# Kernel optimization log

Hardware: AMD Instinct MI355X
Metric: run time of the kernel (lower is better)

## Reference

```python
import jax, jax.numpy as jnp
import numpy as np

TEMPERATURE = 0.8
TOP_K = 50
TOP_P = 0.9
REP_PENALTY = 1.2
NEG_INF = -1000000000.0


def setup_inputs() -> dict:
    key = jax.random.key(0)
    k1, k2 = jax.random.split(key)
    B, S, V, L = 64, 8, 50257, 2048
    logits = jax.random.normal(k1, (B, S, V), dtype=jnp.float32)
    input_ids = jax.random.randint(k2, (B, L), 0, V, dtype=jnp.int64)
    return {"logits": logits, "input_ids": input_ids}


def _modify_logits(logits, input_ids):
    B, S, V = logits.shape
    # temperature scale
    x = logits / TEMPERATURE
    # top-k: keep values >= k-th largest (ties negligible for random floats)
    kth = jax.lax.top_k(x, TOP_K)[0][..., -1:]  # [B,S,1]
    x = jnp.where(x >= kth, x, NEG_INF)
    # top-p nucleus filtering
    order = jnp.argsort(-x, axis=-1)                       # descending order indices
    sorted_logits = jnp.take_along_axis(x, order, axis=-1)
    cum = jnp.cumsum(jax.nn.softmax(sorted_logits, axis=-1), axis=-1)
    remove = cum > TOP_P
    # shift right by one; always keep the top token
    remove = jnp.concatenate([jnp.zeros_like(remove[..., :1]), remove[..., :-1]], axis=-1)
    inv = jnp.argsort(order, axis=-1)                      # inverse permutation
    remove_orig = jnp.take_along_axis(remove, inv, axis=-1)
    x = jnp.where(remove_orig, NEG_INF, x)
    # repetition penalty on last position only, for tokens present in history
    present = jnp.zeros((B, V), dtype=bool).at[
        jnp.arange(B)[:, None], input_ids
    ].set(True)
    last = x[:, -1, :]
    penalized = jnp.where(last < 0, last * REP_PENALTY, last / REP_PENALTY)
    last = jnp.where(present, penalized, last)
    return x.at[:, -1, :].set(last)


def reference(logits, input_ids):
    return _modify_logits(logits, input_ids)
```

## Files before the change

### kernel.cpp

```cpp
#include <hip/hip_runtime.h>
#include <stdint.h>

#define V 50257
#define B_ 64
#define S_ 8
#define ROWS (B_ * S_)
#define L_ 2048
#define NEG_INF -1000000000.0f
#define PEN_NEG (-1200000000.0f)
#define MASK_WORDS_PER_B 1571
#define TOTAL (ROWS * V)
#define NVEC (TOTAL / 4)
#define TOP_CAP 64
#define TRAW 2.8f
#define F4L 7
#define WCHUNK_F4 (64 * F4L)
#define ELEMS_PER_WAVE (WCHUNK_F4 * 4)
#define NWAVES ((NVEC + WCHUNK_F4 - 1) / WCHUNK_F4)
#define GW_BLOCKS ((NWAVES + 3) / 4)
#define WCAP 32
#define CAPROW 512

#define WS_WCNT    0
#define WS_GCAND   65536
#define WS_NEED    (WS_GCAND + (size_t)NWAVES * WCAP * 8)
#define WS_ROWPARAM 0
#define WS_MASK     8192

__device__ __forceinline__ unsigned fkey(float f) {
    unsigned u = __float_as_uint(f);
    return (u & 0x80000000u) ? ~u : (u | 0x80000000u);
}

__device__ __forceinline__ int blockReduceSum256(int v, int tid, int* s4) {
#pragma unroll
    for (int off = 32; off; off >>= 1) v += __shfl_down(v, off);
    __syncthreads();
    if ((tid & 63) == 0) s4[tid >> 6] = v;
    __syncthreads();
    return s4[0] + s4[1] + s4[2] + s4[3];
}


__global__ __launch_bounds__(256) void gather_kernel(const float4* __restrict__ in4,
                                                     uint2* __restrict__ gcand,
                                                     unsigned* __restrict__ wcnt) {
    const int wid = blockIdx.x * 4 + (threadIdx.x >> 6);
    if (wid >= NWAVES) return;
    const int lane = threadIdx.x & 63;
    const int b = wid * WCHUNK_F4 + lane;

    const float4* p0 = in4 + min(b,          NVEC - 1);
    const float4* p1 = in4 + min(b + 64,     NVEC - 1);
    const float4* p2 = in4 + min(b + 2 * 64, NVEC - 1);
    const float4* p3 = in4 + min(b + 3 * 64, NVEC - 1);
    const float4* p4 = in4 + min(b + 4 * 64, NVEC - 1);
    const float4* p5 = in4 + min(b + 5 * 64, NVEC - 1);
    const float4* p6 = in4 + min(b + 6 * 64, NVEC - 1);

    float4 va0, va1, va2, va3, va4, va5, va6;
#define LOADPIN(dst, src)                                                     \
    asm volatile("global_load_dwordx4 %0, %1, off" : "=v"(dst) : "v"(src));   \
    __builtin_amdgcn_sched_barrier(0);
    LOADPIN(va0, p0) LOADPIN(va1, p1) LOADPIN(va2, p2) LOADPIN(va3, p3)
    LOADPIN(va4, p4) LOADPIN(va5, p5) LOADPIN(va6, p6)
#undef LOADPIN
    asm volatile("s_waitcnt vmcnt(0)" ::: "memory");
    __builtin_amdgcn_sched_barrier(0);

    float q0v = 0.f, q1v = 0.f, q2v = 0.f, q3v = 0.f, q4v = 0.f, q5v = 0.f, q6v = 0.f, q7v = 0.f;
    int q0i = 0, q1i = 0, q2i = 0, q3i = 0, q4i = 0, q5i = 0, q6i = 0, q7i = 0;
    int nh = 0;

#define INS(val, ei)                                                          \
    if ((val) >= TRAW) {                                                      \
        q7v = q6v; q7i = q6i; q6v = q5v; q6i = q5i; q5v = q4v; q5i = q4i;     \
        q4v = q3v; q4i = q3i; q3v = q2v; q3i = q2i; q2v = q1v; q2i = q1i;     \
        q1v = q0v; q1i = q0i; q0v = (val); q0i = (ei); ++nh;                  \
    }
#define CONSUME(vv, kk)                                                       \
    {                                                                         \
        int i = b + (kk) * 64;                                                \
        if (i < NVEC) {                                                       \
            int e = i << 2;                                                   \
            INS((vv).x, e)                                                    \
            INS((vv).y, e + 1)                                                \
            INS((vv).z, e + 2)                                                \
            INS((vv).w, e + 3)                                                \
        }                                                                     \
    }
    CONSUME(va0, 0) CONSUME(va1, 1) CONSUME(va2, 2) CONSUME(va3, 3)
    CONSUME(va4, 4) CONSUME(va5, 5) CONSUME(va6, 6)
#undef CONSUME
#undef INS

    int m = nh > 8 ? 8 : nh;
    int incl = m;
#pragma unroll
    for (int d = 1; d < 64; d <<= 1) {
        int t = __shfl_up(incl, d);
        if (lane >= d) incl += t;
    }
    int excl = incl - m;
    int total = __shfl(incl, 63);
    bool of = (total > WCAP) || __any(nh > 8);

    size_t rb = (size_t)wid * WCAP;
    if (m >= 1 && excl + 0 < WCAP) gcand[rb + excl + 0] = make_uint2((unsigned)q0i, __float_as_uint(q0v));
    if (m >= 2 && excl + 1 < WCAP) gcand[rb + excl + 1] = make_uint2((unsigned)q1i, __float_as_uint(q1v));
    if (m >= 3 && excl + 2 < WCAP) gcand[rb + excl + 2] = make_uint2((unsigned)q2i, __float_as_uint(q2v));
    if (m >= 4 && excl + 3 < WCAP) gcand[rb + excl + 3] = make_uint2((unsigned)q3i, __float_as_uint(q3v));
    if (m >= 5 && excl + 4 < WCAP) gcand[rb + excl + 4] = make_uint2((unsigned)q4i, __float_as_uint(q4v));
    if (m >= 6 && excl + 5 < WCAP) gcand[rb + excl + 5] = make_uint2((unsigned)q5i, __float_as_uint(q5v));
    if (m >= 7 && excl + 6 < WCAP) gcand[rb + excl + 6] = make_uint2((unsigned)q6i, __float_as_uint(q6v));
    if (m >= 8 && excl + 7 < WCAP) gcand[rb + excl + 7] = make_uint2((unsigned)q7i, __float_as_uint(q7v));
    if (lane == 0) wcnt[wid] = of ? 1000000u : (unsigned)total;
}


__global__ __launch_bounds__(256) void select_kernel(const float* __restrict__ logits,
                                                     const int* __restrict__ ids,
                                                     const uint2* __restrict__ gcand,
                                                     const unsigned* __restrict__ wcnt,
                                                     float* __restrict__ out) {
    const int row = blockIdx.x;
    const int tid = threadIdx.x;
    __shared__ float cX[CAPROW];
    __shared__ unsigned cR[CAPROW];
    __shared__ int cI[CAPROW];
    __shared__ float sVal[TOP_CAP];
    __shared__ int sIdx[TOP_CAP];
    __shared__ double sExp[TOP_CAP];
    __shared__ unsigned presRow[MASK_WORDS_PER_B];
    __shared__ unsigned s_wc[40];
    __shared__ int s_c, s_M, s_bad, s_ti;
    __shared__ float s_t;
    __shared__ int s_red[4];

    const float* rp = logits + (size_t)row * V;
    const unsigned e0 = (unsigned)row * (unsigned)V;
    if (tid == 0) { s_c = 0; s_bad = 0; }
    __syncthreads();

    {
        const int r0 = (int)(e0 / (unsigned)ELEMS_PER_WAVE);
        const int r1 = (int)((e0 + V - 1) / (unsigned)ELEMS_PER_WAVE);
        const int nr = r1 - r0 + 1;
        if (tid < nr) s_wc[tid] = wcnt[r0 + tid];
        __syncthreads();
        const int nslots = nr * WCAP;
        for (int j = tid; j < nslots; j += 256) {
            int r = j >> 5;
            int sl = j & 31;
            unsigned c = s_wc[r];
            if (c > (unsigned)WCAP) { s_bad = 1; c = WCAP; }
            if (sl < (int)c) {
                uint2 u = gcand[(size_t)(r0 + r) * WCAP + sl];
                if (u.x / (unsigned)V == (unsigned)row) {
                    int p = atomicAdd(&s_c, 1);
                    if (p < CAPROW) {
                        cR[p] = u.y;
                        cX[p] = __uint_as_float(u.y) / 0.8f;
                        cI[p] = (int)(u.x - e0);
                    }
                }
            }
        }
    }
    __syncthreads();
    int cnt = s_c;
    if (s_bad || cnt < 50 || cnt > CAPROW) {
        unsigned lo = 0u, hi = 0xFFFFFFFFu;
        while (lo < hi) {
            unsigned mid = lo + ((hi - lo) >> 1) + 1u;
            int c = 0;
            for (int j = tid; j < V; j += 256) c += (int)(fkey(rp[j]) >= mid);
            c = blockReduceSum256(c, tid, s_red);
            if (c >= 50) lo = mid; else hi = mid - 1u;
        }
        unsigned gl = (lo > 2u) ? lo - 2u : 0u;
        __syncthreads();
        if (tid == 0) s_c = 0;
        __syncthreads();
        for (int j = tid; j < V; j += 256) {
            float v = rp[j];
            if (fkey(v) >= gl) {
                int p = atomicAdd(&s_c, 1);
                if (p < CAPROW) { cR[p] = __float_as_uint(v); cX[p] = v / 0.8f; cI[p] = j; }
            }
        }
        __syncthreads();
        cnt = min(s_c, CAPROW);
    }

    if (tid < TOP_CAP) { sVal[tid] = -3.4e38f; sIdx[tid] = 0x7FFFFFFF; }
    __syncthreads();

    {
        float v0 = -3.4e38f, v1 = -3.4e38f;
        int i0 = 0x7FFFFFFF, i1 = 0x7FFFFFFF;
        if (tid < cnt) { v0 = cX[tid]; i0 = cI[tid]; }
        if (tid + 256 < cnt) { v1 = cX[tid + 256]; i1 = cI[tid + 256]; }
        int r0 = 0, r1 = 0;
        for (int j = 0; j < cnt; ++j) {
            float w = cX[j];
            int wi = cI[j];
            r0 += (w > v0) || (w == v0 && wi < i0);
            r1 += (w > v1) || (w == v1 && wi < i1);
        }
        if (tid < cnt && r0 < TOP_CAP) { sVal[r0] = v0; sIdx[r0] = i0; }
        if (tid + 256 < cnt && r1 < TOP_CAP) { sVal[r1] = v1; sIdx[r1] = i1; }
    }
    __syncthreads();

    if (tid == 0) {
        float kth = sVal[49];
        int M = 50;
        while (M < TOP_CAP && sVal[M] == kth) ++M;
        s_M = M;
    }
    __syncthreads();
    int M = s_M;
    if (tid < M) sExp[tid] = exp((double)sVal[tid] - (double)sVal[0]);
    __syncthreads();
    if (tid == 0) {
        double denom = 0.0;
        for (int i = 0; i < M; ++i) denom += sExp[i];
        double cum = 0.0;
        int J = M - 1;
        for (int i = 0; i < M; ++i) {
            cum += sExp[i] / denom;
            if (cum > 0.9) { J = i; break; }
        }
        s_t = sVal[J];
        s_ti = sIdx[J];
    }

    const bool pen = (row & 7) == 7;
    if (pen) {
        __syncthreads();
        for (int w = tid; w < MASK_WORDS_PER_B; w += 256) presRow[w] = 0u;
        __syncthreads();
        const int* bp = ids + (row >> 3) * L_;
#pragma unroll
        for (int k = 0; k < L_ / 256; ++k) {
            int t = bp[k * 256 + tid];
            atomicOr(&presRow[t >> 5], 1u << (t & 31));
        }
    }
    __syncthreads();

    float* orow = out + (size_t)row * V;
    const unsigned mis = (unsigned)(((size_t)row * (size_t)V) & 3u);
    const int a0 = (int)((4u - mis) & 3u);
    const int nv = (V - a0) >> 2;
    const int tailStart = a0 + (nv << 2);
    if (tid < a0) {
        int t = tid;
        orow[t] = (pen && ((presRow[t >> 5] >> (t & 31)) & 1u)) ? PEN_NEG : NEG_INF;
    }
    if (tid < V - tailStart) {
        int t = tailStart + tid;
        orow[t] = (pen && ((presRow[t >> 5] >> (t & 31)) & 1u)) ? PEN_NEG : NEG_INF;
    }
    float4* ob = reinterpret_cast<float4*>(orow + a0);
    if (!pen) {
        const float4 bg = make_float4(NEG_INF, NEG_INF, NEG_INF, NEG_INF);
        for (int j = tid; j < nv; j += 256) ob[j] = bg;
    } else {
        for (int j = tid; j < nv; j += 256) {
            int t = a0 + (j << 2);
            float4 bg;
            bg.x = ((presRow[t >> 5]     >> (t & 31))     & 1u) ? PEN_NEG : NEG_INF;
            bg.y = ((presRow[(t+1) >> 5] >> ((t+1) & 31)) & 1u) ? PEN_NEG : NEG_INF;
            bg.z = ((presRow[(t+2) >> 5] >> ((t+2) & 31)) & 1u) ? PEN_NEG : NEG_INF;
            bg.w = ((presRow[(t+3) >> 5] >> ((t+3) & 31)) & 1u) ? PEN_NEG : NEG_INF;
            ob[j] = bg;
        }
    }
    __syncthreads();

    float t = s_t;
    int tie = s_ti;
    for (int j = tid; j < cnt; j += 256) {
        float x = cX[j];
        int tok = cI[j];
        bool keep = (x > t) || (x == t && tok <= tie);
        if (keep) {
            float oo = x;
            if (pen && ((presRow[tok >> 5] >> (tok & 31)) & 1u))
                oo = (oo < 0.0f) ? oo * 1.2f : oo * (1.0f / 1.2f);
            orow[tok] = oo;
        }
    }
}

#define CAND_CAP 4096
#define RT_THREADS 1024

__global__ __launch_bounds__(256) void mask_only_kernel(const int* __restrict__ ids,
                                                        unsigned* __restrict__ mask) {
    const int tid = threadIdx.x;
    const int b = blockIdx.x;
    __shared__ unsigned lds[MASK_WORDS_PER_B];
    for (int w = tid; w < MASK_WORDS_PER_B; w += 256) lds[w] = 0u;
    __syncthreads();
    const int* bp = ids + b * L_;
#pragma unroll
    for (int k = 0; k < L_ / 256; ++k) {
        int t = bp[k * 256 + tid];
        atomicOr(&lds[t >> 5], 1u << (t & 31));
    }
    __syncthreads();
    unsigned* mp = mask + b * MASK_WORDS_PER_B;
    for (int w = tid; w < MASK_WORDS_PER_B; w += 256) mp[w] = lds[w];
}

__global__ __launch_bounds__(RT_THREADS, 8) void row_thresh_kernel(
        const float* __restrict__ logits, uint4* __restrict__ rowParam) {
    const int tid = threadIdx.x;
    const int row = blockIdx.x;
    if (row >= ROWS) return;
    const float* rp = logits + (size_t)row * V;

    __shared__ float candV[CAND_CAP];
    __shared__ int   candI[CAND_CAP];
    __shared__ float sVal[TOP_CAP];
    __shared__ int   sIdx[TOP_CAP];
    __shared__ double sExp[TOP_CAP];
    __shared__ int s_cnt, s_M;
    __shared__ int s_red[RT_THREADS / 64];

    const unsigned mis = (unsigned)(((size_t)row * (size_t)V) & 3u);
    const int a0 = (int)((4u - mis) & 3u);
    const int nv = (V - a0) >> 2;
    const int tailStart = a0 + (nv << 2);
    const float4* vp = reinterpret_cast<const float4*>(rp + a0);

    float TR = 2.4f;
    int cnt = 0;
    for (int attempt = 0; attempt < 12; ++attempt) {
        if (tid == 0) s_cnt = 0;
        __syncthreads();
        for (int base = tid; base < nv; base += 4 * RT_THREADS) {
            int i1 = base + RT_THREADS, i2 = base + 2 * RT_THREADS, i3 = base + 3 * RT_THREADS;
            float4 a = vp[base];
            float4 b = vp[i1 < nv ? i1 : nv - 1];
            float4 c = vp[i2 < nv ? i2 : nv - 1];
            float4 d = vp[i3 < nv ? i3 : nv - 1];
            float va[16] = {a.x, a.y, a.z, a.w, b.x, b.y, b.z, b.w,
                            c.x, c.y, c.z, c.w, d.x, d.y, d.z, d.w};
            int ib[4] = {base, i1, i2, i3};
            bool ok[4] = {true, i1 < nv, i2 < nv, i3 < nv};
#pragma unroll
            for (int q = 0; q < 4; ++q) {
                if (!ok[q]) continue;
#pragma unroll
                for (int cc = 0; cc < 4; ++cc) {
                    float v = va[q * 4 + cc];
                    if (v >= TR) {
                        int p = atomicAdd(&s_cnt, 1);
                        if (p < CAND_CAP) { candV[p] = v / 0.8f; candI[p] = a0 + (ib[q] << 2) + cc; }
                    }
                }
            }
        }
        if (tid < a0) {
            float v = rp[tid];
            if (v >= TR) {
                int p = atomicAdd(&s_cnt, 1);
                if (p < CAND_CAP) { candV[p] = v / 0.8f; candI[p] = tid; }
            }
        }
        if (tid < V - tailStart) {
            float v = rp[tailStart + tid];
            if (v >= TR) {
                int p = atomicAdd(&s_cnt, 1);
                if (p < CAND_CAP) { candV[p] = v / 0.8f; candI[p] = tailStart + tid; }
            }
        }
        __syncthreads();
        cnt = s_cnt;
        if (cnt >= 50 && cnt <= CAND_CAP) break;
        if (cnt < 50) TR -= 1.2f; else TR += 1.2f;
        __syncthreads();
    }
    if (cnt > CAND_CAP) cnt = CAND_CAP;

    if (tid < TOP_CAP) { sVal[tid] = -3.4e38f; sIdx[tid] = 0x7FFFFFFF; }
    __syncthreads();

    {
        float v0 = (tid < cnt) ? candV[tid] : -3.4e38f;
        int i0 = (tid < cnt) ? candI[tid] : 0x7FFFFFFF;
        float v1 = (tid + RT_THREADS < cnt) ? candV[tid + RT_THREADS] : -3.4e38f;
        int i1 = (tid + RT_THREADS < cnt) ? candI[tid + RT_THREADS] : 0x7FFFFFFF;
        float v2 = (tid + 2 * RT_THREADS < cnt) ? candV[tid + 2 * RT_THREADS] : -3.4e38f;
        int i2 = (tid + 2 * RT_THREADS < cnt) ? candI[tid + 2 * RT_THREADS] : 0x7FFFFFFF;
        float v3 = (tid + 3 * RT_THREADS < cnt) ? candV[tid + 3 * RT_THREADS] : -3.4e38f;
        int i3 = (tid + 3 * RT_THREADS < cnt) ? candI[tid + 3 * RT_THREADS] : 0x7FFFFFFF;
        int r0 = 0, r1 = 0, r2 = 0, r3 = 0;
        for (int j = 0; j < cnt; ++j) {
            float w = candV[j];
            int wi = candI[j];
            r0 += (w > v0) || (w == v0 && wi < i0);
            r1 += (w > v1) || (w == v1 && wi < i1);
            r2 += (w > v2) || (w == v2 && wi < i2);
            r3 += (w > v3) || (w == v3 && wi < i3);
        }
        if (tid < cnt && r0 < TOP_CAP) { sVal[r0] = v0; sIdx[r0] = i0; }
        if (tid + RT_THREADS < cnt && r1 < TOP_CAP) { sVal[r1] = v1; sIdx[r1] = i1; }
        if (tid + 2 * RT_THREADS < cnt && r2 < TOP_CAP) { sVal[r2] = v2; sIdx[r2] = i2; }
        if (tid + 3 * RT_THREADS < cnt && r3 < TOP_CAP) { sVal[r3] = v3; sIdx[r3] = i3; }
    }
    __syncthreads();

    if (tid == 0) {
        float kth = sVal[49];
        int M = 50;
        while (M < TOP_CAP && sVal[M] == kth) ++M;
        s_M = M;
    }
    __syncthreads();
    int M = s_M;
    if (tid < M) sExp[tid] = exp((double)sVal[tid] - (double)sVal[0]);
    __syncthreads();

    if (tid == 0) {
        double denom = 0.0;
#pragma unroll 1
        for (int i = 0; i < M; ++i) denom += sExp[i];
        double cum = 0.0;
        int J = M - 1;
#pragma unroll 1
        for (int i = 0; i < M; ++i) {
            cum += sExp[i] / denom;
            if (cum > 0.9) { J = i; break; }
        }
        float t = sVal[J];
        float w = t * 0.8f;
        unsigned wb = __float_as_uint(w);
        unsigned lo = 0xFFFFFFFFu, hi = 0u;
        for (int d = -4; d <= 4; ++d) {
            unsigned ub = wb + (unsigned)d;
            if (__uint_as_float(ub) / 0.8f == t) { if (ub < lo) lo = ub; if (ub > hi) hi = ub; }
        }
        rowParam[row] = make_uint4(lo, hi, (unsigned)sIdx[J], 0u);
    }
}

__global__ __launch_bounds__(256) void apply_kernel(const float4* __restrict__ in4,
                                                    const uint4* __restrict__ rowParam,
                                                    const unsigned* __restrict__ mask,
                                                    float4* __restrict__ out4) {
    int gid = blockIdx.x * 256 + threadIdx.x;
    int i0 = gid << 1;
    if (i0 >= NVEC) return;
    float4 a = in4[i0];
    float4 b = in4[i0 + 1];
    unsigned e = (unsigned)i0 << 2;
    unsigned row = e / (unsigned)V;
    unsigned tok0 = e - row * (unsigned)V;
    uint4 p0 = rowParam[row];
    bool crosses = (tok0 + 7u >= (unsigned)V);
    uint4 p1 = crosses ? rowParam[row + 1] : p0;
    float xs[8] = {a.x, a.y, a.z, a.w, b.x, b.y, b.z, b.w};
    float o[8];
#pragma unroll
    for (int c = 0; c < 8; ++c) {
        unsigned tok = tok0 + (unsigned)c;
        unsigned r = row;
        uint4 pp = p0;
        if (tok >= (unsigned)V) { tok -= (unsigned)V; r = row + 1u; pp = p1; }
        float v = xs[c];
        float vlo = __uint_as_float(pp.x);
        float vhi = __uint_as_float(pp.y);
        bool keep = (v > vhi) || (v >= vlo && tok <= pp.z);
        float oo = keep ? v * 1.25f : NEG_INF;
        if ((r & 7u) == 7u) {
            unsigned w = mask[(r >> 3) * MASK_WORDS_PER_B + (tok >> 5)];
            if ((w >> (tok & 31u)) & 1u) oo = (oo < 0.0f) ? oo * 1.2f : oo * (1.0f / 1.2f);
        }
        o[c] = oo;
    }
    out4[i0] = make_float4(o[0], o[1], o[2], o[3]);
    out4[i0 + 1] = make_float4(o[4], o[5], o[6], o[7]);
}

extern "C" void kernel_launch(void* const* d_in, const int* in_sizes, int n_in,
                              void* d_out, int out_size, void* d_ws, size_t ws_size,
                              hipStream_t stream) {
    const float* logits = (const float*)d_in[0];
    const int* ids = (const int*)d_in[1];
    float* out = (float*)d_out;

    if (ws_size >= WS_NEED) {
        unsigned* wcnt = (unsigned*)((char*)d_ws + WS_WCNT);
        uint2* gcand = (uint2*)((char*)d_ws + WS_GCAND);
        gather_kernel<<<GW_BLOCKS, 256, 0, stream>>>((const float4*)logits, gcand, wcnt);
        select_kernel<<<ROWS, 256, 0, stream>>>(logits, ids, gcand, wcnt, out);
    } else {
        uint4* rowParam = (uint4*)((char*)d_ws + WS_ROWPARAM);
        unsigned* mask = (unsigned*)((char*)d_ws + WS_MASK);
        mask_only_kernel<<<B_, 256, 0, stream>>>(ids, mask);
        row_thresh_kernel<<<ROWS, RT_THREADS, 0, stream>>>(logits, rowParam);
        apply_kernel<<<(NVEC / 2 + 255) / 256, 256, 0, stream>>>((const float4*)logits, rowParam,
                                                                 mask, (float4*)out);
    }
}
```

Before: 54.00 us.

## Move background fill into separate flat-grid kernel before select

```diff
diff --git a/kernel.cpp b/kernel.cpp
--- a/kernel.cpp
+++ b/kernel.cpp
@@ -20,6 +20,9 @@
 #define GW_BLOCKS ((NWAVES + 3) / 4)
 #define WCAP 32
 #define CAPROW 512
+#define BG_F4 2048
+#define BG_BLOCKS ((NVEC + BG_F4 - 1) / BG_F4)
+#define BG_PRESW (BG_F4 * 4 / 32)
 
 #define WS_WCNT    0
 #define WS_GCAND   65536
@@ -118,6 +121,59 @@
 }
 
 
+__global__ __launch_bounds__(256) void bg_kernel(const int* __restrict__ ids,
+                                                 float4* __restrict__ out4) {
+    const int blk = blockIdx.x;
+    const int tid = threadIdx.x;
+    const int start = blk * BG_F4;
+    const int end = min(start + BG_F4, NVEC);
+    const unsigned baseE = (unsigned)start << 2;
+    const unsigned endE = (unsigned)end << 2;
+
+    __shared__ unsigned pres[BG_PRESW];
+
+    unsigned r0 = baseE / (unsigned)V, r1 = (endE - 1u) / (unsigned)V;
+    unsigned rl = ((r0 & 7u) == 7u) ? r0 : (((r1 & 7u) == 7u) ? r1 : 0xFFFFFFFFu);
+
+    if (rl == 0xFFFFFFFFu) {
+        const float4 bg = make_float4(NEG_INF, NEG_INF, NEG_INF, NEG_INF);
+#pragma unroll
+        for (int k = 0; k < 8; ++k) {
+            int i = start + tid + k * 256;
+            if (i < end) out4[i] = bg;
+        }
+        return;
+    }
+    for (int w = tid; w < BG_PRESW; w += 256) pres[w] = 0u;
+    __syncthreads();
+    const int* bp = ids + (rl >> 3) * L_;
+    unsigned rowBase = rl * (unsigned)V;
+#pragma unroll
+    for (int k = 0; k < L_ / 256; ++k) {
+        unsigned ge = rowBase + (unsigned)bp[k * 256 + tid];
+        if (ge >= baseE && ge < endE) {
+            unsigned off = ge - baseE;
+            atomicOr(&pres[off >> 5], 1u << (off & 31));
+        }
+    }
+    __syncthreads();
+#pragma unroll
+    for (int k = 0; k < 8; ++k) {
+        int i = start + tid + k * 256;
+        if (i < end) {
+            unsigned off = ((unsigned)i << 2) - baseE;
+            unsigned pw = pres[off >> 5] >> (off & 31u);
+            float4 bg;
+            bg.x = (pw & 1u) ? PEN_NEG : NEG_INF;
+            bg.y = (pw & 2u) ? PEN_NEG : NEG_INF;
+            bg.z = (pw & 4u) ? PEN_NEG : NEG_INF;
+            bg.w = (pw & 8u) ? PEN_NEG : NEG_INF;
+            out4[i] = bg;
+        }
+    }
+}
+
+
 __global__ __launch_bounds__(256) void select_kernel(const float* __restrict__ logits,
                                                      const int* __restrict__ ids,
                                                      const uint2* __restrict__ gcand,
@@ -126,7 +182,6 @@
     const int row = blockIdx.x;
     const int tid = threadIdx.x;
     __shared__ float cX[CAPROW];
-    __shared__ unsigned cR[CAPROW];
     __shared__ int cI[CAPROW];
     __shared__ float sVal[TOP_CAP];
     __shared__ int sIdx[TOP_CAP];
@@ -159,7 +214,6 @@
                 if (u.x / (unsigned)V == (unsigned)row) {
                     int p = atomicAdd(&s_c, 1);
                     if (p < CAPROW) {
-                        cR[p] = u.y;
                         cX[p] = __uint_as_float(u.y) / 0.8f;
                         cI[p] = (int)(u.x - e0);
                     }
@@ -186,7 +240,7 @@
             float v = rp[j];
             if (fkey(v) >= gl) {
                 int p = atomicAdd(&s_c, 1);
-                if (p < CAPROW) { cR[p] = __float_as_uint(v); cX[p] = v / 0.8f; cI[p] = j; }
+                if (p < CAPROW) { cX[p] = v / 0.8f; cI[p] = j; }
             }
         }
         __syncthreads();
@@ -250,38 +304,9 @@
     }
     __syncthreads();
 
-    float* orow = out + (size_t)row * V;
-    const unsigned mis = (unsigned)(((size_t)row * (size_t)V) & 3u);
-    const int a0 = (int)((4u - mis) & 3u);
-    const int nv = (V - a0) >> 2;
-    const int tailStart = a0 + (nv << 2);
-    if (tid < a0) {
-        int t = tid;
-        orow[t] = (pen && ((presRow[t >> 5] >> (t & 31)) & 1u)) ? PEN_NEG : NEG_INF;
-    }
-    if (tid < V - tailStart) {
-        int t = tailStart + tid;
-        orow[t] = (pen && ((presRow[t >> 5] >> (t & 31)) & 1u)) ? PEN_NEG : NEG_INF;
-    }
-    float4* ob = reinterpret_cast<float4*>(orow + a0);
-    if (!pen) {
-        const float4 bg = make_float4(NEG_INF, NEG_INF, NEG_INF, NEG_INF);
-        for (int j = tid; j < nv; j += 256) ob[j] = bg;
-    } else {
-        for (int j = tid; j < nv; j += 256) {
-            int t = a0 + (j << 2);
-            float4 bg;
-            bg.x = ((presRow[t >> 5]     >> (t & 31))     & 1u) ? PEN_NEG : NEG_INF;
-            bg.y = ((presRow[(t+1) >> 5] >> ((t+1) & 31)) & 1u) ? PEN_NEG : NEG_INF;
-            bg.z = ((presRow[(t+2) >> 5] >> ((t+2) & 31)) & 1u) ? PEN_NEG : NEG_INF;
-            bg.w = ((presRow[(t+3) >> 5] >> ((t+3) & 31)) & 1u) ? PEN_NEG : NEG_INF;
-            ob[j] = bg;
-        }
-    }
-    __syncthreads();
-
     float t = s_t;
     int tie = s_ti;
+    float* orow = out + (size_t)row * V;
     for (int j = tid; j < cnt; j += 256) {
         float x = cX[j];
         int tok = cI[j];
@@ -498,6 +523,7 @@
         unsigned* wcnt = (unsigned*)((char*)d_ws + WS_WCNT);
         uint2* gcand = (uint2*)((char*)d_ws + WS_GCAND);
         gather_kernel<<<GW_BLOCKS, 256, 0, stream>>>((const float4*)logits, gcand, wcnt);
+        bg_kernel<<<BG_BLOCKS, 256, 0, stream>>>(ids, (float4*)out);
         select_kernel<<<ROWS, 256, 0, stream>>>(logits, ids, gcand, wcnt, out);
     } else {
         uint4* rowParam = (uint4*)((char*)d_ws + WS_ROWPARAM);
```

New measurement: 58.52 us (median of 2 runs). 8.4% more time.
